# Optimization experiments

Hardware: AMD Instinct MI355X
Metric: run time of the kernel (lower is better)

The kernel has to match this reference:

```python
import jax, jax.numpy as jnp
import numpy as np

B, N, C = 32, 577, 768
H = 12
DH = C // H  # 64
SCALE = DH ** -0.5


def setup_inputs() -> dict:
    key = jax.random.key(0)
    ks = jax.random.split(key, 5)
    x = jax.random.normal(ks[0], (B, N, C), dtype=jnp.float32)
    # Linear params (torch convention: y = x @ W.T + b)
    qkv_w = jax.random.normal(ks[1], (3 * C, C), dtype=jnp.float32) * (C ** -0.5)
    qkv_b = jnp.zeros((3 * C,), dtype=jnp.float32)
    proj_w = jax.random.normal(ks[2], (C, C), dtype=jnp.float32) * (C ** -0.5)
    proj_b = jnp.zeros((C,), dtype=jnp.float32)
    return {"x": x, "qkv_w": qkv_w, "qkv_b": qkv_b, "proj_w": proj_w, "proj_b": proj_b}


def reference(x, qkv_w, qkv_b, proj_w, proj_b):
    b, n, c = x.shape
    qkv = x @ qkv_w.T + qkv_b                       # [B, N, 3C]
    qkv = qkv.reshape(b, n, 3, H, DH).transpose(2, 0, 3, 1, 4)  # [3, B, H, N, DH]
    q, k, v = qkv[0], qkv[1], qkv[2]
    q = q * SCALE
    attn = jnp.einsum('bhnd,bhmd->bhnm', q, k)      # [B, H, N, N]
    # sigmoid -> inverse-sigmoid straight-through rewrite (forward equals logit(sigmoid(attn)))
    sig = jax.nn.sigmoid(attn)
    inv_sig = jnp.log(sig / (1.0 - sig))
    attn_st = attn + jax.lax.stop_gradient(inv_sig - attn)
    p = jax.nn.softmax(attn_st, axis=-1)
    out = jnp.einsum('bhnm,bhmd->bhnd', p, v)       # [B, H, N, DH]
    out = out.transpose(0, 2, 1, 3).reshape(b, n, c)
    return out @ proj_w.T + proj_b
```

## Files before the change

kernel.cpp:

```cpp
#include <hip/hip_runtime.h>

typedef __bf16 bf16;
typedef __attribute__((ext_vector_type(4))) __bf16 bf16x4;
typedef __attribute__((ext_vector_type(8))) __bf16 bf16x8;
typedef __attribute__((ext_vector_type(4))) float f32x4;

#define MFMA_BF16(A_, B_, C_) __builtin_amdgcn_mfma_f32_16x16x32_bf16(A_, B_, C_, 0, 0, 0)

#define BB    32
#define SEQ   577
#define CH    768
#define NH    12
#define DHD   64
#define MROWS (BB * SEQ)
#define NQKV  2304
#define SEQP  584
#define QSCALE 0.1803368801111204f

#define NSTEP 24

__device__ __forceinline__ void async_ld16(const bf16* g, bf16* l) {
  __builtin_amdgcn_global_load_lds(
      (const __attribute__((address_space(1))) void*)g,
      (__attribute__((address_space(3))) void*)l, 16, 0, 0);
}

__global__ __launch_bounds__(256) void cvt_bf16(const float* __restrict__ src,
                                                bf16* __restrict__ dst, int n) {
  int idx = (blockIdx.x * 256 + threadIdx.x) * 4;
  if (idx >= n) return;
  float4 v = *(const float4*)(src + idx);
  bf16x4 o = {(bf16)v.x, (bf16)v.y, (bf16)v.z, (bf16)v.w};
  *(bf16x4*)(dst + idx) = o;
}

__global__ __launch_bounds__(256) void pad_v(bf16* __restrict__ vt) {
  int r = blockIdx.x * 256 + threadIdx.x;
  if (r < BB * NH * DHD) {
    bf16* p = vt + (size_t)r * SEQP + SEQ;
#pragma unroll
    for (int i = 0; i < 7; ++i) p[i] = (bf16)0.f;
  }
}

__global__ __launch_bounds__(256, 2)
void gemm_qkv(const bf16* __restrict__ A, const bf16* __restrict__ W,
              const float* __restrict__ bias,
              bf16* __restrict__ qrm, bf16* __restrict__ krm, bf16* __restrict__ vt) {
  __shared__ bf16 As[2][128 * 32];
  __shared__ bf16 Bs[2][128 * 32];
  const int tid = threadIdx.x, lane = tid & 63, wid = tid >> 6;
  const int quad = lane >> 4, r15 = lane & 15;
  const int m0 = blockIdx.y * 128, n0 = blockIdx.x * 128;
  const int waveM = wid & 1, waveN = wid >> 1;

  const bf16* aSrc[2];
  const bf16* bSrc[2];
  for (int c = 0; c < 2; ++c) {
    int q = wid * 128 + c * 64 + lane;
    int row = q >> 2;
    int sw = (row ^ (row >> 2)) & 3;
    int kc = (q & 3) ^ sw;
    aSrc[c] = A + (size_t)(m0 + row) * CH + kc * 8;
    bSrc[c] = W + (size_t)(n0 + row) * CH + kc * 8;
  }

  f32x4 acc[4][4];
#pragma unroll
  for (int i = 0; i < 4; ++i)
#pragma unroll
    for (int j = 0; j < 4; ++j) acc[i][j] = (f32x4){0.f, 0.f, 0.f, 0.f};

#define GSTAGE(K0, BUF)                                                   \
  {                                                                       \
    _Pragma("unroll") for (int c = 0; c < 2; ++c) {                       \
      async_ld16(aSrc[c] + (K0), &As[BUF][(wid * 128 + c * 64) * 8]);     \
      async_ld16(bSrc[c] + (K0), &Bs[BUF][(wid * 128 + c * 64) * 8]);     \
    }                                                                     \
  }

#define GCOMPUTE(BUF)                                                     \
  {                                                                       \
    bf16x8 af[4], bfr[4];                                                 \
    _Pragma("unroll") for (int s = 0; s < 4; ++s) {                       \
      int rowA = waveM * 64 + s * 16 + r15;                               \
      int ca = quad ^ ((rowA ^ (rowA >> 2)) & 3);                         \
      af[s] = *(const bf16x8*)(&As[BUF][rowA * 32 + ca * 8]);             \
      int rowB = waveN * 64 + s * 16 + r15;                               \
      int cb = quad ^ ((rowB ^ (rowB >> 2)) & 3);                         \
      bfr[s] = *(const bf16x8*)(&Bs[BUF][rowB * 32 + cb * 8]);            \
    }                                                                     \
    _Pragma("unroll") for (int sm = 0; sm < 4; ++sm)                      \
      _Pragma("unroll") for (int sn = 0; sn < 4; ++sn)                    \
        acc[sm][sn] = MFMA_BF16(af[sm], bfr[sn], acc[sm][sn]);            \
  }

  GSTAGE(0, 0);
  for (int k0 = 0; k0 < CH; k0 += 64) {
    __syncthreads();
    GSTAGE(k0 + 32, 1);
    GCOMPUTE(0);
    __syncthreads();
    if (k0 + 64 < CH) GSTAGE(k0 + 64, 0);
    GCOMPUTE(1);
  }

  int t = (n0 >= 1536) ? 2 : (n0 >= 768 ? 1 : 0);
#pragma unroll
  for (int sn = 0; sn < 4; ++sn) {
    int gn = n0 + waveN * 64 + sn * 16 + r15;
    float bv = bias[gn];
    int col = gn - t * CH;
    int h = col >> 6, d = col & 63;
#pragma unroll
    for (int sm = 0; sm < 4; ++sm) {
      int gmBase = m0 + waveM * 64 + sm * 16 + quad * 4;
#pragma unroll
      for (int r = 0; r < 4; ++r) {
        int gm = gmBase + r;
        if (gm < MROWS) {
          float v = acc[sm][sn][r] + bv;
          if (t == 0) {
            qrm[(size_t)gm * CH + col] = (bf16)(v * QSCALE);
          } else if (t == 1) {
            krm[(size_t)gm * CH + col] = (bf16)v;
          } else {
            int b_ = gm / SEQ;
            int n_ = gm - b_ * SEQ;
            vt[((size_t)(b_ * NH + h) * DHD + d) * SEQP + n_] = (bf16)v;
          }
        }
      }
    }
  }
}
#undef GSTAGE
#undef GCOMPUTE

__global__ __launch_bounds__(512, 2)
void gemm_proj(const bf16* __restrict__ A, const bf16* __restrict__ W,
               const float* __restrict__ bias, float* __restrict__ out) {
  __shared__ bf16 As[4][256 * 32];
  __shared__ bf16 Bs[4][256 * 32];
  const int tid = threadIdx.x, lane = tid & 63, wid = tid >> 6;
  const int quad = lane >> 4, r15 = lane & 15;

  const int nbx = (int)gridDim.x;
  const int nwg = nbx * (int)gridDim.y;
  int bid = (int)blockIdx.y * nbx + (int)blockIdx.x;
  int q8 = nwg >> 3, r8 = nwg & 7;
  int xcd = bid & 7, sub = bid >> 3;
  int wg = (xcd < r8 ? xcd * (q8 + 1) : r8 * (q8 + 1) + (xcd - r8) * q8) + sub;
  const int m0 = (wg / nbx) * 256, n0 = (wg % nbx) * 256;

  const int rm = (wid >> 2) * 128;
  const int rn = (wid & 3) * 64;

  int aOff[2], bOff[2];
#pragma unroll
  for (int i = 0; i < 2; ++i) {
    int slot = i * 512 + tid;
    int row = slot >> 2, pc2 = slot & 3;
    int gc2 = pc2 ^ ((row ^ (row >> 2)) & 3);
    aOff[i] = (m0 + row) * CH + gc2 * 8;
    bOff[i] = (n0 + row) * CH + gc2 * 8;
  }

  f32x4 acc[8][4];
#pragma unroll
  for (int i = 0; i < 8; ++i)
#pragma unroll
    for (int j = 0; j < 4; ++j) acc[i][j] = (f32x4){0.f, 0.f, 0.f, 0.f};

#define ISSUE2(S)                                                              \
  {                                                                            \
    const int kb_ = (S) * 32;                                                  \
    const int bf_ = (S) & 3;                                                   \
    _Pragma("unroll") for (int i = 0; i < 2; ++i) {                            \
      async_ld16(A + aOff[i] + kb_, &As[bf_][(i * 512 + tid) * 8]);            \
      async_ld16(W + bOff[i] + kb_, &Bs[bf_][(i * 512 + tid) * 8]);            \
    }                                                                          \
  }

#define COMPUTE2(BF)                                                           \
  {                                                                            \
    bf16x8 bfr[4], afr[8];                                                     \
    _Pragma("unroll") for (int sn = 0; sn < 4; ++sn) {                         \
      int fr = rn + sn * 16 + r15;                                             \
      int pc2 = quad ^ ((fr ^ (fr >> 2)) & 3);                                 \
      bfr[sn] = *(const bf16x8*)(&Bs[BF][fr * 32 + pc2 * 8]);                  \
    }                                                                          \
    _Pragma("unroll") for (int sm = 0; sm < 8; ++sm) {                         \
      int fr = rm + sm * 16 + r15;                                             \
      int pc2 = quad ^ ((fr ^ (fr >> 2)) & 3);                                 \
      afr[sm] = *(const bf16x8*)(&As[BF][fr * 32 + pc2 * 8]);                  \
    }                                                                          \
    _Pragma("unroll") for (int sm = 0; sm < 8; ++sm)                           \
      _Pragma("unroll") for (int sn = 0; sn < 4; ++sn)                         \
        acc[sm][sn] = MFMA_BF16(afr[sm], bfr[sn], acc[sm][sn]);                \
  }

  ISSUE2(0);
  ISSUE2(1);
  for (int s = 0; s < NSTEP; ++s) {
    if (s < NSTEP - 2) {
      ISSUE2(s + 2);
      asm volatile("s_waitcnt vmcnt(8)" ::: "memory");
    } else if (s == NSTEP - 2) {
      asm volatile("s_waitcnt vmcnt(4)" ::: "memory");
    } else {
      asm volatile("s_waitcnt vmcnt(0)" ::: "memory");
    }
    __builtin_amdgcn_s_barrier();
    asm volatile("" ::: "memory");
    COMPUTE2(s & 3);
  }

#pragma unroll
  for (int sn = 0; sn < 4; ++sn) {
    int gn = n0 + rn + sn * 16 + r15;
    float bv = bias[gn];
#pragma unroll
    for (int sm = 0; sm < 8; ++sm) {
      int gmBase = m0 + rm + sm * 16 + quad * 4;
#pragma unroll
      for (int r = 0; r < 4; ++r) {
        int gm = gmBase + r;
        if (gm < MROWS) out[(size_t)gm * CH + gn] = acc[sm][sn][r] + bv;
      }
    }
  }
}
#undef ISSUE2
#undef COMPUTE2

__global__ __launch_bounds__(256, 4)
void attn_kernel(const bf16* __restrict__ qrm, const bf16* __restrict__ krm,
                 const bf16* __restrict__ vt, bf16* __restrict__ ob) {
  __shared__ bf16 Ks[64 * 72];
  __shared__ bf16 Vt[64 * 72];
  __shared__ bf16 Ps[4][2][16 * 72];
  const int tid = threadIdx.x, lane = tid & 63, wid = tid >> 6;
  const int quad = lane >> 4, r15 = lane & 15;
  const int qt = blockIdx.x, bh = blockIdx.y;
  const int b_ = bh / NH, h = bh - b_ * NH;
  const bf16* vtb = vt + (size_t)bh * DHD * SEQP;

  bf16x8 qf[2][2];
#pragma unroll
  for (int g = 0; g < 2; ++g) {
    int qrow = qt * 128 + wid * 32 + g * 16 + r15;
    if (qrow > SEQ - 1) qrow = SEQ - 1;
    const bf16* qp = qrm + (size_t)(b_ * SEQ + qrow) * CH + h * DHD + quad * 8;
    qf[g][0] = *(const bf16x8*)qp;
    qf[g][1] = *(const bf16x8*)(qp + 32);
  }

  f32x4 oacc[2][4];
#pragma unroll
  for (int g = 0; g < 2; ++g)
#pragma unroll
    for (int i = 0; i < 4; ++i) oacc[g][i] = (f32x4){0.f, 0.f, 0.f, 0.f};
  float lrow0 = 0.f, lrow1 = 0.f;

  bf16* P0 = &Ps[wid][0][0];
  bf16* P1 = &Ps[wid][1][0];

  for (int j0 = 0; j0 < SEQ; j0 += 64) {
    __syncthreads();
#pragma unroll
    for (int c = 0; c < 2; ++c) {
      int sid = c * 256 + tid;
      int row = sid >> 3, cc = sid & 7;
      int jr = j0 + row;
      if (jr > SEQ - 1) jr = SEQ - 1;
      *(bf16x8*)(Ks + row * 72 + cc * 8) =
          *(const bf16x8*)(krm + (size_t)(b_ * SEQ + jr) * CH + h * DHD + cc * 8);
      int jst = j0 + cc * 8;
      if (jst > SEQ - 1) jst = SEQ - 1;
      *(bf16x8*)(Vt + row * 72 + cc * 8) = *(const bf16x8*)(vtb + (size_t)row * SEQP + jst);
    }
    __syncthreads();

    f32x4 s0[4], s1[4];
#pragma unroll
    for (int sj = 0; sj < 4; ++sj) {
      bf16x8 kf0 = *(const bf16x8*)(Ks + (sj * 16 + r15) * 72 + quad * 8);
      bf16x8 kf1 = *(const bf16x8*)(Ks + (sj * 16 + r15) * 72 + 32 + quad * 8);
      f32x4 z = (f32x4){0.f, 0.f, 0.f, 0.f};
      s0[sj] = MFMA_BF16(kf0, qf[0][0], z);
      s0[sj] = MFMA_BF16(kf1, qf[0][1], s0[sj]);
      s1[sj] = MFMA_BF16(kf0, qf[1][0], z);
      s1[sj] = MFMA_BF16(kf1, qf[1][1], s1[sj]);
    }

#pragma unroll
    for (int sj = 0; sj < 4; ++sj)
#pragma unroll
      for (int r = 0; r < 4; ++r) {
        int j = j0 + sj * 16 + quad * 4 + r;
        float e0 = (j <= SEQ - 1) ? __builtin_amdgcn_exp2f(s0[sj][r]) : 0.f;
        float e1 = (j <= SEQ - 1) ? __builtin_amdgcn_exp2f(s1[sj][r]) : 0.f;
        s0[sj][r] = e0; lrow0 += e0;
        s1[sj][r] = e1; lrow1 += e1;
      }

#pragma unroll
    for (int sj = 0; sj < 4; ++sj) {
      bf16x4 p0 = {(bf16)s0[sj][0], (bf16)s0[sj][1], (bf16)s0[sj][2], (bf16)s0[sj][3]};
      bf16x4 p1 = {(bf16)s1[sj][0], (bf16)s1[sj][1], (bf16)s1[sj][2], (bf16)s1[sj][3]};
      *(bf16x4*)(P0 + r15 * 72 + sj * 16 + quad * 4) = p0;
      *(bf16x4*)(P1 + r15 * 72 + sj * 16 + quad * 4) = p1;
    }
    asm volatile("s_waitcnt lgkmcnt(0)" ::: "memory");

#pragma unroll
    for (int kc = 0; kc < 2; ++kc) {
      bf16x8 pf0 = *(const bf16x8*)(P0 + r15 * 72 + kc * 32 + quad * 8);
      bf16x8 pf1 = *(const bf16x8*)(P1 + r15 * 72 + kc * 32 + quad * 8);
#pragma unroll
      for (int sd = 0; sd < 4; ++sd) {
        bf16x8 vf = *(const bf16x8*)(Vt + (sd * 16 + r15) * 72 + kc * 32 + quad * 8);
        oacc[0][sd] = MFMA_BF16(pf0, vf, oacc[0][sd]);
        oacc[1][sd] = MFMA_BF16(pf1, vf, oacc[1][sd]);
      }
    }
  }

  lrow0 += __shfl_xor(lrow0, 16);
  lrow0 += __shfl_xor(lrow0, 32);
  lrow1 += __shfl_xor(lrow1, 16);
  lrow1 += __shfl_xor(lrow1, 32);

#pragma unroll
  for (int g = 0; g < 2; ++g) {
    float lr = (g == 0) ? lrow0 : lrow1;
#pragma unroll
    for (int r = 0; r < 4; ++r) {
      int m = quad * 4 + r;
      float rs = __shfl(lr, m);
      int orow = qt * 128 + wid * 32 + g * 16 + m;
      if (orow < SEQ) {
        float inv = 1.0f / rs;
        size_t rowoff = ((size_t)(b_ * SEQ + orow)) * CH + h * DHD;
#pragma unroll
        for (int sd = 0; sd < 4; ++sd)
          ob[rowoff + sd * 16 + r15] = (bf16)(oacc[g][sd][r] * inv);
      }
    }
  }
}

extern "C" void kernel_launch(void* const* d_in, const int* in_sizes, int n_in,
                              void* d_out, int out_size, void* d_ws, size_t ws_size,
                              hipStream_t stream) {
  const float* x      = (const float*)d_in[0];
  const float* qkv_w  = (const float*)d_in[1];
  const float* qkv_b  = (const float*)d_in[2];
  const float* proj_w = (const float*)d_in[3];
  const float* proj_b = (const float*)d_in[4];
  float* out = (float*)d_out;

  char* w = (char*)d_ws;
  bf16* xb  = (bf16*)(w);
  bf16* wqp = (bf16*)(w + 28360704);
  bf16* qrm = (bf16*)(w + 31899648);
  bf16* krm = (bf16*)(w + 60260352);
  bf16* vtb = (bf16*)(w + 88621056);

  cvt_bf16<<<(MROWS * CH / 4 + 255) / 256, 256, 0, stream>>>(x, xb, MROWS * CH);
  cvt_bf16<<<(NQKV * CH / 4 + 255) / 256, 256, 0, stream>>>(qkv_w, wqp, NQKV * CH);
  pad_v<<<(BB * NH * DHD + 255) / 256, 256, 0, stream>>>(vtb);

  gemm_qkv<<<dim3(NQKV / 128, 145), 256, 0, stream>>>(
      xb, wqp, qkv_b, qrm, krm, vtb);

  attn_kernel<<<dim3(5, BB * NH), 256, 0, stream>>>(qrm, krm, vtb, xb);

  cvt_bf16<<<(CH * CH / 4 + 255) / 256, 256, 0, stream>>>(proj_w, wqp, CH * CH);

  gemm_proj<<<dim3(CH / 256, 73), 512, 0, stream>>>(xb, wqp, proj_b, out);
}
```

Measured before the change: 361.2 us.

## Double-buffer attention K/V tiles with async LDS loads and XOR swizzle

The attention kernel now stages K and V tiles through two LDS buffers using global_load_lds. The next 64-key tile is prefetched while the current one is computed, replacing the synchronous global-to-register-to-LDS copy and one of the two barriers per iteration. The LDS layout changes to 32-element rows with an XOR swizzle to avoid bank conflicts, and the occupancy hint drops from 4 to 3 blocks per CU to fit the extra LDS. There is no explicit wait on the async loads before they are read, so correctness depends on the compiler inserting the wait before the barrier.

```diff
diff --git a/kernel.cpp b/kernel.cpp
--- a/kernel.cpp
+++ b/kernel.cpp
@@ -18,6 +18,7 @@
 #define QSCALE 0.1803368801111204f
 
 #define NSTEP 24
+#define NJT   10
 
 __device__ __forceinline__ void async_ld16(const bf16* g, bf16* l) {
   __builtin_amdgcn_global_load_lds(
@@ -234,17 +235,43 @@
 #undef ISSUE2
 #undef COMPUTE2
 
-__global__ __launch_bounds__(256, 4)
+__global__ __launch_bounds__(256, 3)
 void attn_kernel(const bf16* __restrict__ qrm, const bf16* __restrict__ krm,
                  const bf16* __restrict__ vt, bf16* __restrict__ ob) {
-  __shared__ bf16 Ks[64 * 72];
-  __shared__ bf16 Vt[64 * 72];
+  __shared__ bf16 Ks[2][128 * 32];
+  __shared__ bf16 Vt[2][128 * 32];
   __shared__ bf16 Ps[4][2][16 * 72];
   const int tid = threadIdx.x, lane = tid & 63, wid = tid >> 6;
   const int quad = lane >> 4, r15 = lane & 15;
   const int qt = blockIdx.x, bh = blockIdx.y;
   const int b_ = bh / NH, h = bh - b_ * NH;
   const bf16* vtb = vt + (size_t)bh * DHD * SEQP;
+  const bf16* krmb = krm + (size_t)b_ * SEQ * CH + h * DHD;
+
+  int jloc_[2], off_[2];
+  const bf16* vrow_[2];
+#pragma unroll
+  for (int c = 0; c < 2; ++c) {
+    int q = wid * 128 + c * 64 + lane;
+    int hr = q >> 2;
+    int kc = (q & 3) ^ ((hr ^ (hr >> 2)) & 3);
+    jloc_[c] = hr >> 1;
+    off_[c] = (hr & 1) * 32 + kc * 8;
+    vrow_[c] = vtb + (size_t)(hr >> 1) * SEQP;
+  }
+
+#define ASTAGE(J0, BUF)                                                        \
+  {                                                                            \
+    _Pragma("unroll") for (int c = 0; c < 2; ++c) {                            \
+      int jr = (J0) + jloc_[c];                                                \
+      if (jr > SEQ - 1) jr = SEQ - 1;                                          \
+      async_ld16(krmb + (size_t)jr * CH + off_[c],                             \
+                 &Ks[BUF][(wid * 128 + c * 64) * 8]);                          \
+      int js = (J0) + off_[c];                                                 \
+      if (js > SEQ - 1) js = SEQ - 1;                                          \
+      async_ld16(vrow_[c] + js, &Vt[BUF][(wid * 128 + c * 64) * 8]);           \
+    }                                                                          \
+  }
 
   bf16x8 qf[2][2];
 #pragma unroll
@@ -266,27 +293,21 @@
   bf16* P0 = &Ps[wid][0][0];
   bf16* P1 = &Ps[wid][1][0];
 
-  for (int j0 = 0; j0 < SEQ; j0 += 64) {
+  ASTAGE(0, 0);
+  int buf = 0;
+  for (int t = 0; t < NJT; ++t) {
+    const int j0 = t * 64;
     __syncthreads();
-#pragma unroll
-    for (int c = 0; c < 2; ++c) {
-      int sid = c * 256 + tid;
-      int row = sid >> 3, cc = sid & 7;
-      int jr = j0 + row;
-      if (jr > SEQ - 1) jr = SEQ - 1;
-      *(bf16x8*)(Ks + row * 72 + cc * 8) =
-          *(const bf16x8*)(krm + (size_t)(b_ * SEQ + jr) * CH + h * DHD + cc * 8);
-      int jst = j0 + cc * 8;
-      if (jst > SEQ - 1) jst = SEQ - 1;
-      *(bf16x8*)(Vt + row * 72 + cc * 8) = *(const bf16x8*)(vtb + (size_t)row * SEQP + jst);
-    }
-    __syncthreads();
+    if (t + 1 < NJT) ASTAGE(j0 + 64, buf ^ 1);
 
     f32x4 s0[4], s1[4];
 #pragma unroll
     for (int sj = 0; sj < 4; ++sj) {
-      bf16x8 kf0 = *(const bf16x8*)(Ks + (sj * 16 + r15) * 72 + quad * 8);
-      bf16x8 kf1 = *(const bf16x8*)(Ks + (sj * 16 + r15) * 72 + 32 + quad * 8);
+      int hr0 = (sj * 16 + r15) * 2, hr1 = hr0 + 1;
+      int p0c = quad ^ ((hr0 ^ (hr0 >> 2)) & 3);
+      int p1c = quad ^ ((hr1 ^ (hr1 >> 2)) & 3);
+      bf16x8 kf0 = *(const bf16x8*)(&Ks[buf][hr0 * 32 + p0c * 8]);
+      bf16x8 kf1 = *(const bf16x8*)(&Ks[buf][hr1 * 32 + p1c * 8]);
       f32x4 z = (f32x4){0.f, 0.f, 0.f, 0.f};
       s0[sj] = MFMA_BF16(kf0, qf[0][0], z);
       s0[sj] = MFMA_BF16(kf1, qf[0][1], s0[sj]);
@@ -320,12 +341,16 @@
       bf16x8 pf1 = *(const bf16x8*)(P1 + r15 * 72 + kc * 32 + quad * 8);
 #pragma unroll
       for (int sd = 0; sd < 4; ++sd) {
-        bf16x8 vf = *(const bf16x8*)(Vt + (sd * 16 + r15) * 72 + kc * 32 + quad * 8);
+        int hrv = (sd * 16 + r15) * 2 + kc;
+        int pv = quad ^ ((hrv ^ (hrv >> 2)) & 3);
+        bf16x8 vf = *(const bf16x8*)(&Vt[buf][hrv * 32 + pv * 8]);
         oacc[0][sd] = MFMA_BF16(pf0, vf, oacc[0][sd]);
         oacc[1][sd] = MFMA_BF16(pf1, vf, oacc[1][sd]);
       }
     }
-  }
+    buf ^= 1;
+  }
+#undef ASTAGE
 
   lrow0 += __shfl_xor(lrow0, 16);
   lrow0 += __shfl_xor(lrow0, 32);
```

Result: faster. 350.3 us (-3.0%).
